# Kernel optimization log

Hardware: AMD Instinct MI355X
Metric: run time of the kernel (lower is better)

Reference implementation:

```python
import jax, jax.numpy as jnp
import numpy as np
from jax import lax

N = 2048
B = 8
CH = 10
START = 1
STOP = 65


def setup_inputs() -> dict:
    key = jax.random.key(0)
    ks = jax.random.split(key, 13)

    def g(k, s):
        return jax.random.normal(k, s, jnp.float32) * 0.05

    return {
        "x": jax.random.normal(ks[0], (B, 1, N, N), jnp.float32),
        "wl": g(ks[1], (CH // 2, 1, 3, N)), "bl": g(ks[2], (CH // 2,)),
        "wr": g(ks[3], (CH // 2, 1, N, 3)), "br": g(ks[4], (CH // 2,)),
        "wA": g(ks[5], (CH, CH, 3)), "bA": g(ks[6], (CH,)),
        "wB": g(ks[7], (CH, CH, 3)), "bB": g(ks[8], (CH,)),  # shared by layers 2&3 (torch list aliasing)
        "wT": g(ks[9], (CH, CH, 3)), "bT": g(ks[10], (CH,)),
        "wm": g(ks[11], (2, CH, 1)), "bm": g(ks[12], (2,)),
        "start": START, "stop": STOP,
    }


def _conv1d(h, w, b, pad):
    y = lax.conv_general_dilated(h, w, (1,), [(pad, pad)], dimension_numbers=("NCH", "OIH", "NCH"))
    return y + b[None, :, None]


def _forward(x, wl, bl, wr, br, wA, bA, wB, bB, wT, bT, wm, bm, start, stop):
    n = x.shape[-1]
    # scan_left: Conv2d kernel (3, n), padding (1, 0) -> (B, 5, n, 1) -> squeeze
    left_ = lax.conv_general_dilated(x, wl, (1, 1), [(1, 1), (0, 0)], dimension_numbers=("NCHW", "OIHW", "NCHW"))
    left_ = left_[..., 0] + bl[None, :, None]
    # scan_right: Conv2d kernel (n, 3), padding (0, 1) -> (B, 5, 1, n) -> squeeze
    right_ = lax.conv_general_dilated(x, wr, (1, 1), [(0, 0), (1, 1)], dimension_numbers=("NCHW", "OIHW", "NCHW"))
    right_ = right_[:, :, 0, :] + br[None, :, None]
    lr = jnp.concatenate([left_, right_], axis=1)  # (B, 10, n)
    h = jax.nn.relu(_conv1d(lr, wA, bA, 1))
    h = jax.nn.relu(_conv1d(h, wB, bB, 1))  # same weights twice: torch [conv, relu]*2 aliasing
    h = jax.nn.relu(_conv1d(h, wB, bB, 1))
    # ConvTranspose1d(k=3, stride=1, pad=1) == Conv1d with transposed, spatially-flipped kernel, pad=1
    wTc = jnp.flip(jnp.swapaxes(wT, 0, 1), -1)
    for _ in range(3):
        h = jax.nn.relu(_conv1d(h, wTc, bT, 1))
    m = jax.nn.sigmoid(_conv1d(h, wm, bm, 0))  # (B, 2, n)
    left, right = m[:, 0, :], m[:, 1, :]
    xs = x[:, 0]  # (B, n, n)
    preds = []
    for d in range(start, stop):  # static diagonal indices
        curr = jnp.exp(jnp.diagonal(xs, offset=d, axis1=1, axis2=2))  # (B, n-d)
        mass_in = curr[:, 1:] * right[:, 1:n - d] + curr[:, :-1] * left[:, d:n - 1]
        mass_out = right[:, 0:n - d - 1] + left[:, d + 1:n]
        p = jnp.log(mass_in / mass_out)
        preds.append(p - jnp.mean(p))  # scalar mean over batch+positions, as torch.mean
    return jnp.concatenate(preds, axis=1)  # ragged preds concatenated: (B, sum(n-d-1))


def reference(x, wl, bl, wr, br, wA, bA, wB, bB, wT, bT, wm, bm, start, stop):
    return _forward(x, wl, bl, wr, br, wA, bA, wB, bB, wT, bT, wm, bm, start, stop)
```

## Files before the change

kernel.cpp:

```cpp
#include <hip/hip_runtime.h>
#include <hip/hip_bf16.h>

#define NN 2048
#define BB 8
#define TROW 128928

__global__ __launch_bounds__(256) void k_left(const float* __restrict__ x,
                                              const float* __restrict__ wl,
                                              float* __restrict__ R) {
    __shared__ float red[4][60 * 65];
    int b = blockIdx.x >> 7;
    int rbase = (blockIdx.x & 127) << 4;
    int wv = threadIdx.x >> 6, lane = threadIdx.x & 63;
    int r0 = rbase + wv * 4;
    const float* xp = x + ((size_t)(b * NN + r0)) * NN;

    float acc[4][15];
#pragma unroll
    for (int r = 0; r < 4; r++)
#pragma unroll
        for (int k = 0; k < 15; k++) acc[r][k] = 0.f;

    for (int seg = 0; seg < 8; seg++) {
        int j0 = seg * 256 + lane * 4;
        float4 xv[4];
#pragma unroll
        for (int r = 0; r < 4; r++) xv[r] = *(const float4*)(xp + (size_t)r * NN + j0);
#pragma unroll
        for (int k = 0; k < 15; k++) {
            float4 w4 = *(const float4*)(wl + (size_t)k * NN + j0);
#pragma unroll
            for (int r = 0; r < 4; r++) {
                acc[r][k] = fmaf(xv[r].x, w4.x, acc[r][k]);
                acc[r][k] = fmaf(xv[r].y, w4.y, acc[r][k]);
                acc[r][k] = fmaf(xv[r].z, w4.z, acc[r][k]);
                acc[r][k] = fmaf(xv[r].w, w4.w, acc[r][k]);
            }
        }
    }
#pragma unroll
    for (int r = 0; r < 4; r++)
#pragma unroll
        for (int k = 0; k < 15; k++) red[wv][(r * 15 + k) * 65 + lane] = acc[r][k];
    __syncthreads();
    if (lane < 60) {
        const float* rp = &red[wv][lane * 65];
        float s = 0.f;
#pragma unroll
        for (int j = 0; j < 64; j++) s += rp[j];
        int r = lane / 15, k = lane - r * 15;
        R[(size_t)(b * NN + r0 + r) * 16 + k] = s;
    }
}

__global__ __launch_bounds__(256) void k_prep(const float* __restrict__ wr,
                                              float* __restrict__ WF) {
    int t = blockIdx.x * 256 + threadIdx.x;
    if (t >= NN * 16) return;
    int h = t >> 4, k = t & 15;
    float v = 0.f;
    if (k < 15) {
        int c = k / 3, dw = k - c * 3;
        v = wr[c * (NN * 3) + h * 3 + dw];
    }
    WF[t] = v;
}

__global__ __launch_bounds__(512) void k_right(const float* __restrict__ x,
                                               const float* __restrict__ WF,
                                               float* __restrict__ CSp) {
    __shared__ float wf[512 * 16];
    __shared__ float CS_l[15 * 256];
    int b = blockIdx.x >> 5;
    int rem = blockIdx.x & 31;
    int jc = rem >> 2, rc = rem & 3;
    int j0 = jc * 256, r0 = rc * 512;
    int tid = threadIdx.x;
    int wv = tid >> 6, lane = tid & 63;

#pragma unroll
    for (int s = 0; s < 16; s++) {
        int vi = s * 512 + tid;
        if (vi < 2048) *(((float4*)wf) + vi) = *(((const float4*)(WF + (size_t)r0 * 16)) + vi);
    }
    for (int idx = tid; idx < 15 * 256; idx += 512) CS_l[idx] = 0.f;
    __syncthreads();

    float acc[15][4];
#pragma unroll
    for (int k = 0; k < 15; k++)
#pragma unroll
        for (int e = 0; e < 4; e++) acc[k][e] = 0.f;

    const float* xp = x + ((size_t)b * NN + r0) * NN + j0 + lane * 4;
#pragma unroll 2
    for (int i = 0; i < 64; i++) {
        int rloc = wv + 8 * i;
        float4 xv = *(const float4*)(xp + (size_t)rloc * NN);
        const float* wrow = &wf[rloc * 16];
        float4 w0 = *(const float4*)(wrow);
        float4 w1 = *(const float4*)(wrow + 4);
        float4 w2 = *(const float4*)(wrow + 8);
        float4 w3 = *(const float4*)(wrow + 12);
        float wk[15] = {w0.x, w0.y, w0.z, w0.w, w1.x, w1.y, w1.z, w1.w,
                        w2.x, w2.y, w2.z, w2.w, w3.x, w3.y, w3.z};
#pragma unroll
        for (int k = 0; k < 15; k++) {
            acc[k][0] = fmaf(xv.x, wk[k], acc[k][0]);
            acc[k][1] = fmaf(xv.y, wk[k], acc[k][1]);
            acc[k][2] = fmaf(xv.z, wk[k], acc[k][2]);
            acc[k][3] = fmaf(xv.w, wk[k], acc[k][3]);
        }
    }
    int l4 = lane * 4;
#pragma unroll
    for (int k = 0; k < 15; k++)
#pragma unroll
        for (int e = 0; e < 4; e++) atomicAdd(&CS_l[k * 256 + l4 + e], acc[k][e]);
    __syncthreads();
    float* outp = CSp + (((size_t)rc * BB + b) * 16) * NN + j0;
    for (int idx = tid; idx < 15 * 256; idx += 512) {
        int k = idx >> 8, col = idx & 255;
        outp[(size_t)k * NN + col] = CS_l[idx];
    }
}

__global__ __launch_bounds__(256) void k_combine(const float* __restrict__ R,
                                                 const float* __restrict__ CSp,
                                                 const float* __restrict__ bl,
                                                 const float* __restrict__ br,
                                                 float* __restrict__ LR) {
    int t = blockIdx.x * 256 + threadIdx.x;
    if (t >= BB * 10 * NN) return;
    int b = t / (10 * NN);
    int rem = t - b * (10 * NN);
    int ch = rem >> 11;
    int i = rem & (NN - 1);
    float v;
    if (ch < 5) {
        v = bl[ch];
#pragma unroll
        for (int dh = 0; dh < 3; dh++) {
            int r = i + dh - 1;
            if (r >= 0 && r < NN) v += R[(size_t)(b * NN + r) * 16 + ch * 3 + dh];
        }
    } else {
        int c = ch - 5;
        v = br[c];
#pragma unroll
        for (int dw = 0; dw < 3; dw++) {
            int j = i + dw - 1;
            if (j >= 0 && j < NN) {
#pragma unroll
                for (int rc = 0; rc < 4; rc++)
                    v += CSp[(((size_t)rc * BB + b) * 16 + c * 3 + dw) * NN + j];
            }
        }
    }
    LR[t] = v;
}

__global__ __launch_bounds__(256) void k_chain(const float* __restrict__ LR,
                                               const float* __restrict__ wA, const float* __restrict__ bA,
                                               const float* __restrict__ wB, const float* __restrict__ bB,
                                               const float* __restrict__ wT, const float* __restrict__ bT,
                                               const float* __restrict__ wm, const float* __restrict__ bm,
                                               float* __restrict__ LEFT, float* __restrict__ RIGHT) {
    __shared__ float buf0[10][144], buf1[10][144];
    __shared__ float W[3][10][10][3];
    __shared__ float Bs[3][10];
    __shared__ float Wm[2][10], Bm[2];
    int b = blockIdx.x >> 4;
    int c0 = (blockIdx.x & 15) << 7;
    int tid = threadIdx.x;

    for (int idx = tid; idx < 900; idx += 256) {
        int set = idx / 300, rem = idx - set * 300;
        int o = rem / 30, rem2 = rem - o * 30, c = rem2 / 3, kk = rem2 - c * 3;
        float u;
        if (set == 0) u = wA[o * 30 + c * 3 + kk];
        else if (set == 1) u = wB[o * 30 + c * 3 + kk];
        else u = wT[c * 30 + o * 3 + (2 - kk)];
        W[set][o][c][kk] = u;
    }
    if (tid < 30) {
        float v = (tid < 10) ? bA[tid] : (tid < 20) ? bB[tid - 10] : bT[tid - 20];
        Bs[tid / 10][tid % 10] = v;
    }
    if (tid < 20) Wm[tid / 10][tid % 10] = wm[tid];
    if (tid < 2) Bm[tid] = bm[tid];

    for (int idx = tid; idx < 1400; idx += 256) {
        int ch = idx / 140, p = idx - ch * 140;
        int g = c0 - 6 + p;
        buf0[ch][p] = (g >= 0 && g < NN) ? LR[((size_t)b * 10 + ch) * NN + g] : 0.f;
    }
    __syncthreads();

    float(*in)[144] = buf0;
    float(*out)[144] = buf1;
    for (int layer = 0; layer < 6; layer++) {
        int set = (layer == 0) ? 0 : (layer < 3 ? 1 : 2);
        int lo = layer + 1;
        for (int idx = tid; idx < 1400; idx += 256) {
            int o = idx / 140, p = idx - o * 140;
            if (p >= lo && p < 140 - lo) {
                float s = Bs[set][o];
#pragma unroll
                for (int c = 0; c < 10; c++) {
                    const float* ip = &in[c][p];
                    s = fmaf(ip[-1], W[set][o][c][0], s);
                    s = fmaf(ip[0], W[set][o][c][1], s);
                    s = fmaf(ip[1], W[set][o][c][2], s);
                }
                s = s > 0.f ? s : 0.f;
                int g = c0 - 6 + p;
                if (g < 0 || g >= NN) s = 0.f;
                out[o][p] = s;
            }
        }
        __syncthreads();
        float(*tmp)[144] = in; in = out; out = tmp;
    }
    {
        int idx = tid;
        int o = idx >> 7, pp = idx & 127;
        int p = 6 + pp;
        float s = Bm[o];
#pragma unroll
        for (int c = 0; c < 10; c++) s = fmaf(in[c][p], Wm[o][c], s);
        float sig = 1.f / (1.f + __expf(-s));
        (o ? RIGHT : LEFT)[b * NN + c0 + pp] = sig;
    }
}

__global__ __launch_bounds__(256) void k_diag(const float* __restrict__ x,
                                              float* __restrict__ CUR) {
    __shared__ float T[64][65];
    int b = blockIdx.x >> 5;
    int i0 = (blockIdx.x & 31) << 6;
    int tid = threadIdx.x;
    int rsub = tid >> 3, chunk = tid & 7;
#pragma unroll
    for (int rh = 0; rh < 2; rh++) {
        int rr = rsub + rh * 32;
        int row = i0 + rr;
        const float* xp = x + ((size_t)b * NN + row) * NN;
#pragma unroll
        for (int j = 0; j < 8; j++) {
            int d = chunk * 8 + j + 1;
            int col = row + d;
            float v = 0.f;
            if (col < NN) v = __expf(xp[col]);
            T[rr][d - 1] = v;
        }
    }
    __syncthreads();
    int lane = tid & 63, dgrp = tid >> 6;
#pragma unroll
    for (int sub = 0; sub < 16; sub++) {
        int dm1 = dgrp * 16 + sub;
        CUR[((size_t)dm1 * BB + b) * NN + i0 + lane] = T[lane][dm1];
    }
}

__global__ __launch_bounds__(1024) void k_mass(const float* __restrict__ CUR,
                                               const float* __restrict__ LEFT,
                                               const float* __restrict__ RIGHT,
                                               float* __restrict__ P,
                                               float* __restrict__ psum) {
    __shared__ float wsum[16];
    int dm1 = blockIdx.x >> 2, q = blockIdx.x & 3;
    int d = dm1 + 1;
    int L = (NN - 1) - d;
    int tid = threadIdx.x;
    int b2 = tid >> 9, ii = tid & 511;
    int i = q * 512 + ii;
    float lsum = 0.f;
#pragma unroll
    for (int bs = 0; bs < 4; bs++) {
        int b = b2 + bs * 2;
        float p = 0.f;
        if (i < L) {
            const float* cur = CUR + ((size_t)dm1 * BB + b) * NN;
            const float* lf = LEFT + b * NN;
            const float* rt = RIGHT + b * NN;
            float mi = cur[i + 1] * rt[i + 1] + cur[i] * lf[d + i];
            float mo = rt[i] + lf[d + 1 + i];
            p = __logf(mi / mo);
            lsum += p;
            P[((size_t)dm1 * BB + b) * NN + i] = p;
        }
    }
    for (int off = 32; off; off >>= 1) lsum += __shfl_down(lsum, off);
    int lane = tid & 63, wv = tid >> 6;
    if (lane == 0) wsum[wv] = lsum;
    __syncthreads();
    if (wv == 0) {
        float s = (lane < 16) ? wsum[lane] : 0.f;
        for (int off = 8; off; off >>= 1) s += __shfl_down(s, off);
        if (lane == 0) atomicAdd(&psum[dm1], s);
    }
}

__global__ __launch_bounds__(1024) void k_out(const float* __restrict__ P,
                                              const float* __restrict__ psum,
                                              float* __restrict__ outp) {
    int dm1 = blockIdx.x >> 2, q = blockIdx.x & 3;
    int d = dm1 + 1;
    int L = (NN - 1) - d;
    int tid = threadIdx.x;
    int b2 = tid >> 9, ii = tid & 511;
    int i = q * 512 + ii;
    if (i >= L) return;
    float mean = psum[dm1] / (float)(8 * L);
    size_t off0 = (size_t)dm1 * (NN - 1) - (size_t)dm1 * (dm1 + 1) / 2;
#pragma unroll
    for (int bs = 0; bs < 4; bs++) {
        int b = b2 + bs * 2;
        outp[(size_t)b * TROW + off0 + i] = P[((size_t)dm1 * BB + b) * NN + i] - mean;
    }
}

extern "C" void kernel_launch(void* const* d_in, const int* in_sizes, int n_in,
                              void* d_out, int out_size, void* d_ws, size_t ws_size,
                              hipStream_t stream) {
    const float* x = (const float*)d_in[0];
    const float* wl = (const float*)d_in[1];
    const float* bl = (const float*)d_in[2];
    const float* wr = (const float*)d_in[3];
    const float* br = (const float*)d_in[4];
    const float* wA = (const float*)d_in[5];
    const float* bA = (const float*)d_in[6];
    const float* wB = (const float*)d_in[7];
    const float* bB = (const float*)d_in[8];
    const float* wT = (const float*)d_in[9];
    const float* bT = (const float*)d_in[10];
    const float* wm = (const float*)d_in[11];
    const float* bm = (const float*)d_in[12];

    float* ws = (float*)d_ws;
    float* R    = ws;
    float* CSp  = ws + 262144;
    float* WF   = ws + 1310720;
    float* LR   = ws + 1343488;
    float* LEFT = ws + 1507328;
    float* RIGHT= ws + 1523712;
    float* CUR  = ws + 1540096;
    float* P    = ws + 2588672;
    float* psum = ws + 3637248;

    hipMemsetAsync(psum, 0, 64 * sizeof(float), stream);
    k_left<<<1024, 256, 0, stream>>>(x, wl, R);
    k_prep<<<128, 256, 0, stream>>>(wr, WF);
    k_right<<<256, 512, 0, stream>>>(x, WF, CSp);
    k_combine<<<640, 256, 0, stream>>>(R, CSp, bl, br, LR);
    k_chain<<<128, 256, 0, stream>>>(LR, wA, bA, wB, bB, wT, bT, wm, bm, LEFT, RIGHT);
    k_diag<<<256, 256, 0, stream>>>(x, CUR);
    k_mass<<<256, 1024, 0, stream>>>(CUR, LEFT, RIGHT, P, psum);
    k_out<<<256, 1024, 0, stream>>>(P, psum, (float*)d_out);
}
```

Measured before the change: 335.8 us.

## Fuse prep, combine, diag and mass stages to cut launches and intermediates

Folds the weight-repack kernel into k_right, the combine step into the conv chain's shared-memory load, and the diagonal-extract kernel into the mass computation so the diagonals stay in shared memory instead of going through a CUR buffer. The psum memset moves into k_left. This removes four launches and the global round-trips for WF, LR and CUR. In exchange the chain kernel recomputes halo values, k_right does scattered weight loads, and the diagonal reads from x in k_diagmass are strided.

```diff
diff --git a/kernel.cpp b/kernel.cpp
--- a/kernel.cpp
+++ b/kernel.cpp
@@ -7,7 +7,9 @@
 
 __global__ __launch_bounds__(256) void k_left(const float* __restrict__ x,
                                               const float* __restrict__ wl,
-                                              float* __restrict__ R) {
+                                              float* __restrict__ R,
+                                              float* __restrict__ psum) {
+    if (blockIdx.x == 0 && threadIdx.x < 64) psum[threadIdx.x] = 0.f;
     __shared__ float red[4][60 * 65];
     int b = blockIdx.x >> 7;
     int rbase = (blockIdx.x & 127) << 4;
@@ -53,21 +55,8 @@
     }
 }
 
-__global__ __launch_bounds__(256) void k_prep(const float* __restrict__ wr,
-                                              float* __restrict__ WF) {
-    int t = blockIdx.x * 256 + threadIdx.x;
-    if (t >= NN * 16) return;
-    int h = t >> 4, k = t & 15;
-    float v = 0.f;
-    if (k < 15) {
-        int c = k / 3, dw = k - c * 3;
-        v = wr[c * (NN * 3) + h * 3 + dw];
-    }
-    WF[t] = v;
-}
-
 __global__ __launch_bounds__(512) void k_right(const float* __restrict__ x,
-                                               const float* __restrict__ WF,
+                                               const float* __restrict__ wr,
                                                float* __restrict__ CSp) {
     __shared__ float wf[512 * 16];
     __shared__ float CS_l[15 * 256];
@@ -78,10 +67,10 @@
     int tid = threadIdx.x;
     int wv = tid >> 6, lane = tid & 63;
 
-#pragma unroll
-    for (int s = 0; s < 16; s++) {
-        int vi = s * 512 + tid;
-        if (vi < 2048) *(((float4*)wf) + vi) = *(((const float4*)(WF + (size_t)r0 * 16)) + vi);
+    for (int idx = tid; idx < 512 * 15; idx += 512) {
+        int hh = idx / 15, k = idx - hh * 15;
+        int c = k / 3, dw = k - c * 3;
+        wf[hh * 16 + k] = wr[c * (NN * 3) + (r0 + hh) * 3 + dw];
     }
     for (int idx = tid; idx < 15 * 256; idx += 512) CS_l[idx] = 0.f;
     __syncthreads();
@@ -125,47 +114,15 @@
     }
 }
 
-__global__ __launch_bounds__(256) void k_combine(const float* __restrict__ R,
-                                                 const float* __restrict__ CSp,
-                                                 const float* __restrict__ bl,
-                                                 const float* __restrict__ br,
-                                                 float* __restrict__ LR) {
-    int t = blockIdx.x * 256 + threadIdx.x;
-    if (t >= BB * 10 * NN) return;
-    int b = t / (10 * NN);
-    int rem = t - b * (10 * NN);
-    int ch = rem >> 11;
-    int i = rem & (NN - 1);
-    float v;
-    if (ch < 5) {
-        v = bl[ch];
-#pragma unroll
-        for (int dh = 0; dh < 3; dh++) {
-            int r = i + dh - 1;
-            if (r >= 0 && r < NN) v += R[(size_t)(b * NN + r) * 16 + ch * 3 + dh];
-        }
-    } else {
-        int c = ch - 5;
-        v = br[c];
-#pragma unroll
-        for (int dw = 0; dw < 3; dw++) {
-            int j = i + dw - 1;
-            if (j >= 0 && j < NN) {
-#pragma unroll
-                for (int rc = 0; rc < 4; rc++)
-                    v += CSp[(((size_t)rc * BB + b) * 16 + c * 3 + dw) * NN + j];
-            }
-        }
-    }
-    LR[t] = v;
-}
-
-__global__ __launch_bounds__(256) void k_chain(const float* __restrict__ LR,
-                                               const float* __restrict__ wA, const float* __restrict__ bA,
-                                               const float* __restrict__ wB, const float* __restrict__ bB,
-                                               const float* __restrict__ wT, const float* __restrict__ bT,
-                                               const float* __restrict__ wm, const float* __restrict__ bm,
-                                               float* __restrict__ LEFT, float* __restrict__ RIGHT) {
+__global__ __launch_bounds__(256) void k_chainC(const float* __restrict__ R,
+                                                const float* __restrict__ CSp,
+                                                const float* __restrict__ bl,
+                                                const float* __restrict__ br,
+                                                const float* __restrict__ wA, const float* __restrict__ bA,
+                                                const float* __restrict__ wB, const float* __restrict__ bB,
+                                                const float* __restrict__ wT, const float* __restrict__ bT,
+                                                const float* __restrict__ wm, const float* __restrict__ bm,
+                                                float* __restrict__ LEFT, float* __restrict__ RIGHT) {
     __shared__ float buf0[10][144], buf1[10][144];
     __shared__ float W[3][10][10][3];
     __shared__ float Bs[3][10];
@@ -193,7 +150,30 @@
     for (int idx = tid; idx < 1400; idx += 256) {
         int ch = idx / 140, p = idx - ch * 140;
         int g = c0 - 6 + p;
-        buf0[ch][p] = (g >= 0 && g < NN) ? LR[((size_t)b * 10 + ch) * NN + g] : 0.f;
+        float v = 0.f;
+        if (g >= 0 && g < NN) {
+            if (ch < 5) {
+                v = bl[ch];
+#pragma unroll
+                for (int dh = 0; dh < 3; dh++) {
+                    int r = g + dh - 1;
+                    if (r >= 0 && r < NN) v += R[(size_t)(b * NN + r) * 16 + ch * 3 + dh];
+                }
+            } else {
+                int c = ch - 5;
+                v = br[c];
+#pragma unroll
+                for (int dw = 0; dw < 3; dw++) {
+                    int j = g + dw - 1;
+                    if (j >= 0 && j < NN) {
+#pragma unroll
+                        for (int rc = 0; rc < 4; rc++)
+                            v += CSp[(((size_t)rc * BB + b) * 16 + c * 3 + dw) * NN + j];
+                    }
+                }
+            }
+        }
+        buf0[ch][p] = v;
     }
     __syncthreads();
 
@@ -234,73 +214,49 @@
     }
 }
 
-__global__ __launch_bounds__(256) void k_diag(const float* __restrict__ x,
-                                              float* __restrict__ CUR) {
-    __shared__ float T[64][65];
+__global__ __launch_bounds__(256) void k_diagmass(const float* __restrict__ x,
+                                                  const float* __restrict__ LEFT,
+                                                  const float* __restrict__ RIGHT,
+                                                  float* __restrict__ P,
+                                                  float* __restrict__ psum) {
+    __shared__ float T[65][65];
+    __shared__ float psl[64];
     int b = blockIdx.x >> 5;
     int i0 = (blockIdx.x & 31) << 6;
     int tid = threadIdx.x;
-    int rsub = tid >> 3, chunk = tid & 7;
-#pragma unroll
-    for (int rh = 0; rh < 2; rh++) {
-        int rr = rsub + rh * 32;
-        int row = i0 + rr;
-        const float* xp = x + ((size_t)b * NN + row) * NN;
-#pragma unroll
-        for (int j = 0; j < 8; j++) {
-            int d = chunk * 8 + j + 1;
-            int col = row + d;
-            float v = 0.f;
-            if (col < NN) v = __expf(xp[col]);
-            T[rr][d - 1] = v;
-        }
-    }
-    __syncthreads();
-    int lane = tid & 63, dgrp = tid >> 6;
-#pragma unroll
-    for (int sub = 0; sub < 16; sub++) {
-        int dm1 = dgrp * 16 + sub;
-        CUR[((size_t)dm1 * BB + b) * NN + i0 + lane] = T[lane][dm1];
-    }
-}
-
-__global__ __launch_bounds__(1024) void k_mass(const float* __restrict__ CUR,
-                                               const float* __restrict__ LEFT,
-                                               const float* __restrict__ RIGHT,
-                                               float* __restrict__ P,
-                                               float* __restrict__ psum) {
-    __shared__ float wsum[16];
-    int dm1 = blockIdx.x >> 2, q = blockIdx.x & 3;
-    int d = dm1 + 1;
-    int L = (NN - 1) - d;
-    int tid = threadIdx.x;
-    int b2 = tid >> 9, ii = tid & 511;
-    int i = q * 512 + ii;
-    float lsum = 0.f;
-#pragma unroll
-    for (int bs = 0; bs < 4; bs++) {
-        int b = b2 + bs * 2;
+
+    for (int idx = tid; idx < 65 * 64; idx += 256) {
+        int r = idx >> 6, dm1 = idx & 63;
+        int row = i0 + r;
+        int col = row + dm1 + 1;
+        float v = 0.f;
+        if (row < NN && col < NN) v = __expf(x[((size_t)b * NN + row) * NN + col]);
+        T[r][dm1] = v;
+    }
+    __syncthreads();
+
+    int wv = tid >> 6, lane = tid & 63;
+    int i = i0 + lane;
+    const float* lf = LEFT + b * NN;
+    const float* rt = RIGHT + b * NN;
+#pragma unroll
+    for (int s = 0; s < 16; s++) {
+        int dm1 = wv * 16 + s;
+        int d = dm1 + 1;
+        int L = (NN - 1) - d;
         float p = 0.f;
         if (i < L) {
-            const float* cur = CUR + ((size_t)dm1 * BB + b) * NN;
-            const float* lf = LEFT + b * NN;
-            const float* rt = RIGHT + b * NN;
-            float mi = cur[i + 1] * rt[i + 1] + cur[i] * lf[d + i];
+            float mi = T[lane + 1][dm1] * rt[i + 1] + T[lane][dm1] * lf[d + i];
             float mo = rt[i] + lf[d + 1 + i];
             p = __logf(mi / mo);
-            lsum += p;
             P[((size_t)dm1 * BB + b) * NN + i] = p;
         }
-    }
-    for (int off = 32; off; off >>= 1) lsum += __shfl_down(lsum, off);
-    int lane = tid & 63, wv = tid >> 6;
-    if (lane == 0) wsum[wv] = lsum;
-    __syncthreads();
-    if (wv == 0) {
-        float s = (lane < 16) ? wsum[lane] : 0.f;
-        for (int off = 8; off; off >>= 1) s += __shfl_down(s, off);
-        if (lane == 0) atomicAdd(&psum[dm1], s);
-    }
+        float s64 = p;
+        for (int off = 32; off; off >>= 1) s64 += __shfl_down(s64, off);
+        if (lane == 0) psl[dm1] = s64;
+    }
+    __syncthreads();
+    if (tid < 64) atomicAdd(&psum[tid], psl[tid]);
 }
 
 __global__ __launch_bounds__(1024) void k_out(const float* __restrict__ P,
@@ -342,21 +298,14 @@
     float* ws = (float*)d_ws;
     float* R    = ws;
     float* CSp  = ws + 262144;
-    float* WF   = ws + 1310720;
-    float* LR   = ws + 1343488;
-    float* LEFT = ws + 1507328;
-    float* RIGHT= ws + 1523712;
-    float* CUR  = ws + 1540096;
-    float* P    = ws + 2588672;
-    float* psum = ws + 3637248;
-
-    hipMemsetAsync(psum, 0, 64 * sizeof(float), stream);
-    k_left<<<1024, 256, 0, stream>>>(x, wl, R);
-    k_prep<<<128, 256, 0, stream>>>(wr, WF);
-    k_right<<<256, 512, 0, stream>>>(x, WF, CSp);
-    k_combine<<<640, 256, 0, stream>>>(R, CSp, bl, br, LR);
-    k_chain<<<128, 256, 0, stream>>>(LR, wA, bA, wB, bB, wT, bT, wm, bm, LEFT, RIGHT);
-    k_diag<<<256, 256, 0, stream>>>(x, CUR);
-    k_mass<<<256, 1024, 0, stream>>>(CUR, LEFT, RIGHT, P, psum);
+    float* LEFT = ws + 1310720;
+    float* RIGHT= ws + 1327104;
+    float* P    = ws + 1343488;
+    float* psum = ws + 2392064;
+
+    k_left<<<1024, 256, 0, stream>>>(x, wl, R, psum);
+    k_right<<<256, 512, 0, stream>>>(x, wr, CSp);
+    k_chainC<<<128, 256, 0, stream>>>(R, CSp, bl, br, wA, bA, wB, bB, wT, bT, wm, bm, LEFT, RIGHT);
+    k_diagmass<<<256, 256, 0, stream>>>(x, LEFT, RIGHT, P, psum);
     k_out<<<256, 1024, 0, stream>>>(P, psum, (float*)d_out);
 }
```

New measurement: 346.4 us. 1.03x slower.
